# Performance work log

Hardware: AMD Instinct MI355X
Metric: run time of the kernel (lower is better)

The kernel has to match this reference:

```python
import jax, jax.numpy as jnp
import numpy as np
from jax.scipy.special import logsumexp

B, D, H, L, R, K = 4096, 784, 16, 4, 4, 8
D1 = D // 2
NBIS, NNEWT = 50, 3
LOG2PI = float(np.log(2.0 * np.pi))


def square_swish(h):
    # util.square_swish nonlinearity (swish-family; see notes)
    return h * jax.nn.sigmoid(h)


def mixture_terms(xv, logits, mu, log_s):
    # xv: [B, D1]; logits/mu/log_s: [B, D1, K]
    logw = jax.nn.log_softmax(logits, axis=-1)
    t = (xv[..., None] - mu) * jnp.exp(-log_s)
    log_cdf = logsumexp(logw + jax.nn.log_sigmoid(t), axis=-1)          # log F(x)
    log_sf = logsumexp(logw + jax.nn.log_sigmoid(-t), axis=-1)          # log (1-F(x))
    log_pdf = logsumexp(logw + jax.nn.log_sigmoid(t) + jax.nn.log_sigmoid(-t) - log_s, axis=-1)  # log F'(x)
    return log_cdf, log_sf, log_pdf


def invert_mixture_logit(y, logits, mu, log_s):
    # Solve logit(F(x)) = y for x: bisection (stop-grad) + Newton polish (differentiable).
    sl, sm, ss, sy = map(jax.lax.stop_gradient, (logits, mu, log_s, y))

    def body(_, lo_hi):
        lo, hi = lo_hi
        mid = 0.5 * (lo + hi)
        lc, lsf, _ = mixture_terms(mid, sl, sm, ss)
        f = lc - lsf - sy
        return jnp.where(f < 0, mid, lo), jnp.where(f < 0, hi, mid)

    lo = jnp.full_like(y, -100.0)
    hi = jnp.full_like(y, 100.0)
    lo, hi = jax.lax.fori_loop(0, NBIS, body, (lo, hi))
    xv = jax.lax.stop_gradient(0.5 * (lo + hi))
    for _ in range(NNEWT):
        lc, lsf, lp = mixture_terms(xv, logits, mu, log_s)
        logdet = lp - lc - lsf  # d/dx logit(F(x))
        xv = xv - (lc - lsf - y) * jnp.exp(-logdet)
    lc, lsf, lp = mixture_terms(xv, logits, mu, log_s)
    return xv, lp - lc - lsf


def conditioner(h_in, Wi, bi, W1l, b1l, W2l, b2l, Wo, bo):
    h = square_swish(h_in @ Wi + bi)
    for r in range(R):  # 4 resnet blocks, hidden_dim=16
        h = h + square_swish(h @ W1l[r] + b1l[r]) @ W2l[r] + b2l[r]
    return (h @ Wo + bo).reshape(-1, D1, 3 * K)


def flow_inverse(x, eps, W_in, b_in, W1, b1, W2, b2, W_out, b_out):
    # UnitGaussianPrior sample eps -> inverse coupling stack; log q via change of variables
    log_q = -0.5 * jnp.sum(eps * eps + LOG2PI, axis=-1)
    z = eps
    for l in reversed(range(L)):
        za, zb = z[:, :D1], z[:, D1:]
        if l % 2 == 1:
            za, zb = zb, za
        p = conditioner(jnp.concatenate([zb, x], axis=-1),
                        W_in[l], b_in[l], W1[l], b1[l], W2[l], b2[l], W_out[l], b_out[l])
        logits, mu, log_s = p[..., :K], p[..., K:2 * K], p[..., 2 * K:]
        xa, ld = invert_mixture_logit(za, logits, mu, log_s)
        log_q = log_q + jnp.sum(ld, axis=-1)
        if l % 2 == 0:
            z = jnp.concatenate([xa, zb], axis=-1)
        else:
            z = jnp.concatenate([zb, xa], axis=-1)
    return z, log_q


def setup_inputs():
    key = jax.random.key(0)
    ks = jax.random.split(key, 6)
    s_in = 1.0 / np.sqrt(D1 + D)
    s_h = 1.0 / np.sqrt(H)
    return {
        "x": jax.random.normal(ks[0], (B, D), jnp.float32),
        "eps": jax.random.normal(ks[1], (B, D), jnp.float32),
        "W_in": jax.random.normal(ks[2], (L, D1 + D, H), jnp.float32) * s_in,
        "b_in": jnp.zeros((L, H), jnp.float32),
        "W1": jax.random.normal(ks[3], (L, R, H, H), jnp.float32) * s_h,
        "b1": jnp.zeros((L, R, H), jnp.float32),
        "W2": jax.random.normal(ks[4], (L, R, H, H), jnp.float32) * s_h,
        "b2": jnp.zeros((L, R, H), jnp.float32),
        "W_out": jax.random.normal(ks[5], (L, H, D1 * 3 * K), jnp.float32) * 0.05,
        "b_out": jnp.zeros((L, D1 * 3 * K), jnp.float32),
    }


def reference(x, eps, W_in, b_in, W1, b1, W2, b2, W_out, b_out):
    return flow_inverse(x, eps, W_in, b_in, W1, b1, W2, b2, W_out, b_out)
```

## Files before the change

### kernel.cpp

```cpp
#include <hip/hip_runtime.h>
#include <math.h>

constexpr int cB   = 4096;
constexpr int cD   = 784;
constexpr int cD1  = 392;
constexpr int cH   = 16;
constexpr int cL   = 4;
constexpr int cR   = 4;
constexpr int cDIN = 1176;
constexpr int cPDIM = cD1 * 3 * 8;
#define LOG2PI_F 1.8378770664093453f
#define L2E_F    1.4426950408889634f
#define LN2_F    0.6931471805599453f
#define LN_LN2_F (-0.36651292058166432701f)

__device__ __forceinline__ float rcpf(float x)  { return __builtin_amdgcn_rcpf(x); }
__device__ __forceinline__ float exp2f_(float x){ return __builtin_amdgcn_exp2f(x); }
__device__ __forceinline__ float log2f_(float x){ return __builtin_amdgcn_logf(x); }
__device__ __forceinline__ float expn(float x)  { return exp2f_(x * L2E_F); }
__device__ __forceinline__ float logn(float x)  { return log2f_(x) * LN2_F; }

typedef __attribute__((ext_vector_type(2))) float f32x2;

__global__ void __launch_bounds__(256, 4) mlp_kernel(
    const float* __restrict__ zbsrc, const float* __restrict__ x,
    const float* __restrict__ Win, const float* __restrict__ bin,
    const float* __restrict__ W1, const float* __restrict__ b1,
    const float* __restrict__ W2, const float* __restrict__ b2,
    float* __restrict__ hbuf,
    const float* __restrict__ eps, float* __restrict__ logq, int do_init)
{
    __shared__ float part[4][4][16];
    const int wid  = threadIdx.x >> 6;
    const int lane = threadIdx.x & 63;
    const int j = lane & 15;
    const int G = lane >> 4;
    const int bs = blockIdx.x * 4;
    const int r0 = wid * 294;

    if (do_init) {
        const int b = bs + wid;
        const float4* e = (const float4*)(eps + (size_t)b * cD);
        float sum = 0.f;
        for (int i = lane; i < cD / 4; i += 64) {
            float4 v = e[i];
            sum = fmaf(v.x, v.x, sum); sum = fmaf(v.y, v.y, sum);
            sum = fmaf(v.z, v.z, sum); sum = fmaf(v.w, v.w, sum);
        }
        #pragma unroll
        for (int off = 32; off; off >>= 1) sum += __shfl_xor(sum, off, 64);
        if (lane == 0) logq[b] = -0.5f * sum - 0.5f * (float)cD * LOG2PI_F;
    }

    float acc[4][16];
    #pragma unroll
    for (int s = 0; s < 4; ++s)
        #pragma unroll
        for (int c = 0; c < 16; ++c) acc[s][c] = 0.f;

    const float* pz[4]; const float* px[4];
    #pragma unroll
    for (int s = 0; s < 4; ++s) {
        pz[s] = zbsrc + (size_t)(bs + s) * cD;
        px[s] = x + (size_t)(bs + s) * cD - cD1;
    }

    for (int i = r0 + lane; i < r0 + 294; i += 64) {
        const float4* wr = (const float4*)(Win + (size_t)i * cH);
        float4 w0 = wr[0], w1 = wr[1], w2 = wr[2], w3 = wr[3];
        float wv[16] = {w0.x,w0.y,w0.z,w0.w, w1.x,w1.y,w1.z,w1.w,
                        w2.x,w2.y,w2.z,w2.w, w3.x,w3.y,w3.z,w3.w};
        #pragma unroll
        for (int s = 0; s < 4; ++s) {
            const float* src = (i < cD1) ? pz[s] : px[s];
            float v = src[i];
            #pragma unroll
            for (int c = 0; c < 16; ++c) acc[s][c] = fmaf(v, wv[c], acc[s][c]);
        }
    }

    #pragma unroll
    for (int s = 0; s < 4; ++s) {
        #pragma unroll
        for (int c = 0; c < 8; ++c) {
            float sent = (lane & 8) ? acc[s][c] : acc[s][c + 8];
            float mine = (lane & 8) ? acc[s][c + 8] : acc[s][c];
            acc[s][c] = mine + __shfl_xor(sent, 8, 64);
        }
        #pragma unroll
        for (int c = 0; c < 4; ++c) {
            float sent = (lane & 4) ? acc[s][c] : acc[s][c + 4];
            float mine = (lane & 4) ? acc[s][c + 4] : acc[s][c];
            acc[s][c] = mine + __shfl_xor(sent, 4, 64);
        }
        #pragma unroll
        for (int c = 0; c < 2; ++c) {
            float sent = (lane & 2) ? acc[s][c] : acc[s][c + 2];
            float mine = (lane & 2) ? acc[s][c + 2] : acc[s][c];
            acc[s][c] = mine + __shfl_xor(sent, 2, 64);
        }
        {
            float sent = (lane & 1) ? acc[s][0] : acc[s][1];
            float mine = (lane & 1) ? acc[s][1] : acc[s][0];
            acc[s][0] = mine + __shfl_xor(sent, 1, 64);
        }
    }
    const int g4 = (lane >> 4) & 1, g5 = (lane >> 5) & 1;
    float a01, a23, colsum;
    {
        float sent = g4 ? acc[0][0] : acc[1][0];
        float keep = g4 ? acc[1][0] : acc[0][0];
        a01 = keep + __shfl_xor(sent, 16, 64);
    }
    {
        float sent = g4 ? acc[2][0] : acc[3][0];
        float keep = g4 ? acc[3][0] : acc[2][0];
        a23 = keep + __shfl_xor(sent, 16, 64);
    }
    {
        float sent = g5 ? a01 : a23;
        float keep = g5 ? a23 : a01;
        colsum = keep + __shfl_xor(sent, 32, 64);
    }

    part[wid][G][j] = colsum;
    __syncthreads();
    if (wid != 0) return;

    colsum = part[0][G][j] + part[1][G][j] + part[2][G][j] + part[3][G][j];

    float t0 = colsum + bin[j];
    float hj = t0 * rcpf(1.0f + expn(-t0));

    #pragma unroll
    for (int r = 0; r < cR; ++r) {
        const float* w1r = W1 + r * 256;
        const float* w2r = W2 + r * 256;
        float u = b1[r * 16 + j];
        #pragma unroll
        for (int i = 0; i < 16; ++i)
            u = fmaf(__shfl(hj, i, 16), w1r[i * 16 + j], u);
        u = u * rcpf(1.0f + expn(-u));
        float v = b2[r * 16 + j];
        #pragma unroll
        for (int i = 0; i < 16; ++i)
            v = fmaf(__shfl(u, i, 16), w2r[i * 16 + j], v);
        hj += v;
    }
    hbuf[(size_t)j * cB + (bs + G)] = hj;
}

__global__ void __launch_bounds__(256) invert_kernel(
    float* __restrict__ z, const float* __restrict__ ysrc,
    const float* __restrict__ hbuf,
    const float* __restrict__ Wo, const float* __restrict__ bo,
    float* __restrict__ logq, int za_off)
{
    const int wid  = threadIdx.x >> 6;
    const int lane = threadIdx.x & 63;
    const int d = __builtin_amdgcn_readfirstlane(blockIdx.x * 4 + wid);
    const int b = blockIdx.y * 64 + lane;

    float hh[16];
    #pragma unroll
    for (int i = 0; i < 16; ++i) hh[i] = hbuf[(size_t)i * cB + b];

    f32x2 P[12];
    {
        const f32x2* bp = (const f32x2*)(bo + (size_t)d * 24);
        #pragma unroll
        for (int j2 = 0; j2 < 12; ++j2) P[j2] = bp[j2];
        #pragma unroll
        for (int i = 0; i < 16; ++i) {
            float hv = hh[i];
            f32x2 hv2 = {hv, hv};
            const f32x2* wr = (const f32x2*)(Wo + (size_t)i * cPDIM + (size_t)d * 24);
            #pragma unroll
            for (int j2 = 0; j2 < 12; ++j2)
                P[j2] = __builtin_elementwise_fma(hv2, wr[j2], P[j2]);
        }
    }
    float p[24];
    #pragma unroll
    for (int j2 = 0; j2 < 12; ++j2) { p[2*j2] = P[j2].x; p[2*j2+1] = P[j2].y; }

    const float y0  = ysrc[(size_t)b * cD + za_off + d];
    const float sgn = (y0 < 0.f) ? -1.f : 1.f;
    const float yb  = fabsf(y0);

    float wt[8], pm[8], q2[8], is2[8], nm2[8], wis2[8];
    float S, lgSn, SLN2, lo, hi, x0;
    {
        float m = p[0];
        #pragma unroll
        for (int k = 1; k < 8; ++k) m = fmaxf(m, p[k]);
        S = 0.f;
        #pragma unroll
        for (int k = 0; k < 8; ++k) {
            pm[k] = p[k] - m;
            wt[k] = exp2f_(pm[k] * L2E_F);
            S += wt[k];
        }
        lgSn = log2f_(S) * LN2_F;
        SLN2 = S * LN2_F;
        float lo0 = 1e30f, hi0 = -1e30f, xa = 0.f;
        #pragma unroll
        for (int k = 0; k < 8; ++k) {
            q2[k] = p[16 + k] * L2E_F;
            float sk  = exp2f_(q2[k]);
            float ik  = exp2f_(-q2[k]);
            is2[k] = ik * L2E_F;
            float mub = sgn * p[8 + k];
            nm2[k] = -mub * is2[k];
            wis2[k] = wt[k] * is2[k];
            float inv = fmaf(yb, sk, mub);
            lo0 = fminf(lo0, inv); hi0 = fmaxf(hi0, inv);
            xa = fmaf(wt[k], inv, xa);
        }
        float pad = 1e-3f + 1e-5f * (fabsf(lo0) + fabsf(hi0));
        lo = lo0 - pad; hi = hi0 + pad;
        x0 = xa * rcpf(S);
    }

    f32x2 wt2[4], is22[4], nm22[4], wis22[4];
    #pragma unroll
    for (int kk = 0; kk < 4; ++kk) {
        wt2[kk]   = (f32x2){wt[2*kk],   wt[2*kk+1]};
        is22[kk]  = (f32x2){is2[2*kk],  is2[2*kk+1]};
        nm22[kk]  = (f32x2){nm2[2*kk],  nm2[2*kk+1]};
        wis22[kk] = (f32x2){wis2[2*kk], wis2[2*kk+1]};
    }

    float xv, ld;
    if (yb <= 30.0f) {
        xv = x0;
        #pragma unroll 1
        for (int it = 0; it < 3; ++it) {
            f32x2 xv2 = {xv, xv};
            f32x2 sfv2 = {0.f, 0.f}, pdfa2 = {0.f, 0.f};
            #pragma unroll
            for (int kk = 0; kk < 4; ++kk) {
                f32x2 t2 = __builtin_elementwise_fma(xv2, is22[kk], nm22[kk]);
                f32x2 e1;
                e1.x = 1.0f + exp2f_(t2.x);
                e1.y = 1.0f + exp2f_(t2.y);
                f32x2 r = { rcpf(e1.x), rcpf(e1.y) };
                sfv2  = __builtin_elementwise_fma(wt2[kk], r, sfv2);
                f32x2 rr = __builtin_elementwise_fma(-r, r, r);
                pdfa2 = __builtin_elementwise_fma(wis22[kk], rr, pdfa2);
            }
            float sfv = sfv2.x + sfv2.y;
            float pdfa = pdfa2.x + pdfa2.y;
            float cdf = S - sfv;
            float f = (log2f_(cdf) - log2f_(sfv)) * LN2_F;
            if (f < yb) lo = xv; else hi = xv;
            float step = (f - yb) * cdf * sfv * rcpf(pdfa * SLN2);
            float xn = xv - step;
            if (!(xn > lo && xn < hi)) xn = 0.5f * (lo + hi);
            xv = xn;
        }
        {
            f32x2 xv2 = {xv, xv};
            f32x2 sfv2 = {0.f, 0.f}, pdfa2 = {0.f, 0.f};
            #pragma unroll
            for (int kk = 0; kk < 4; ++kk) {
                f32x2 t2 = __builtin_elementwise_fma(xv2, is22[kk], nm22[kk]);
                f32x2 e1;
                e1.x = 1.0f + exp2f_(t2.x);
                e1.y = 1.0f + exp2f_(t2.y);
                f32x2 r = { rcpf(e1.x), rcpf(e1.y) };
                sfv2  = __builtin_elementwise_fma(wt2[kk], r, sfv2);
                f32x2 rr = __builtin_elementwise_fma(-r, r, r);
                pdfa2 = __builtin_elementwise_fma(wis22[kk], rr, pdfa2);
            }
            float sfv = sfv2.x + sfv2.y;
            float pdfa = pdfa2.x + pdfa2.y;
            float cdf = S - sfv;
            float l2c = log2f_(cdf), l2s = log2f_(sfv), l2p = log2f_(pdfa);
            ld = (l2p - l2c - l2s) * LN2_F + LN_LN2_F + lgSn;
            float f = (l2c - l2s) * LN2_F;
            if (f < yb) lo = xv; else hi = xv;
            float step = (f - yb) * cdf * sfv * rcpf(pdfa * SLN2);
            float xn = xv - step;
            if (!(xn > lo && xn < hi)) xn = 0.5f * (lo + hi);
            xv = xn;
        }
    } else {
        float lw[8], lis[8];
        #pragma unroll
        for (int k = 0; k < 8; ++k) {
            lw[k]  = pm[k] - lgSn;
            lis[k] = -q2[k] * LN2_F;
        }
        xv = x0;
        #pragma unroll 1
        for (int it = 0; it < 4; ++it) {
            float u[8];
            float mu_ = -1e30f;
            #pragma unroll
            for (int k = 0; k < 8; ++k) {
                float t  = fmaf(xv, is2[k], nm2[k]) * LN2_F;
                float ec = fminf(expn(-t), 1.0f);
                u[k] = lw[k] - t - ec * fmaf(-0.5f, ec, 1.0f);
                mu_ = fmaxf(mu_, u[k]);
            }
            float Su = 0.f;
            #pragma unroll
            for (int k = 0; k < 8; ++k) Su += expn(u[k] - mu_);
            float lsf = mu_ + logn(Su);
            float m2 = -1e30f;
            #pragma unroll
            for (int k = 0; k < 8; ++k) m2 = fmaxf(m2, u[k] + lis[k]);
            float S2 = 0.f;
            #pragma unroll
            for (int k = 0; k < 8; ++k) S2 += expn(u[k] + lis[k] - m2);
            float lp = m2 + logn(S2);
            if (it == 3) { ld = lp - lsf; break; }
            float f = -lsf;
            if (f < yb) lo = xv; else hi = xv;
            float step = (f - yb) * expn(lsf - lp);
            float xn = xv - step;
            if (!(xn > lo && xn < hi)) xn = 0.5f * (lo + hi);
            xv = xn;
        }
    }

    z[(size_t)b * cD + za_off + d] = sgn * xv;

    __shared__ float red[256];
    red[threadIdx.x] = ld;
    __syncthreads();
    if (wid == 0) {
        float ssum = red[lane] + red[lane + 64] + red[lane + 128] + red[lane + 192];
        atomicAdd(&logq[b], ssum);
    }
}

extern "C" void kernel_launch(void* const* d_in, const int* in_sizes, int n_in,
                              void* d_out, int out_size, void* d_ws, size_t ws_size,
                              hipStream_t stream) {
    const float* x     = (const float*)d_in[0];
    const float* eps   = (const float*)d_in[1];
    const float* W_in  = (const float*)d_in[2];
    const float* b_in  = (const float*)d_in[3];
    const float* W1    = (const float*)d_in[4];
    const float* b1    = (const float*)d_in[5];
    const float* W2    = (const float*)d_in[6];
    const float* b2    = (const float*)d_in[7];
    const float* W_out = (const float*)d_in[8];
    const float* b_out = (const float*)d_in[9];

    float* z    = (float*)d_out;
    float* logq = z + (size_t)cB * cD;
    float* hbuf = (float*)d_ws;

    for (int l = cL - 1; l >= 0; --l) {
        const int zb_off = (l & 1) ? 0 : cD1;
        const int za_off = (l & 1) ? cD1 : 0;
        const float* zbsrc = (l == 3) ? (eps + zb_off) : (z + zb_off);
        const float* ysrc  = (l >= 2) ? eps : z;
        mlp_kernel<<<cB / 4, 256, 0, stream>>>(
            zbsrc, x,
            W_in + (size_t)l * cDIN * cH, b_in + (size_t)l * cH,
            W1 + (size_t)l * cR * cH * cH, b1 + (size_t)l * cR * cH,
            W2 + (size_t)l * cR * cH * cH, b2 + (size_t)l * cR * cH,
            hbuf,
            eps, logq, (l == 3) ? 1 : 0);
        invert_kernel<<<dim3(cD1 / 4, cB / 64), 256, 0, stream>>>(
            z, ysrc, hbuf,
            W_out + (size_t)l * cH * cPDIM, b_out + (size_t)l * cPDIM,
            logq, za_off);
    }
}
```

Measured before the change: 290.7 us.

## Stage Wo tile and hidden activations in shared memory for invert kernel

The invert kernel now loads the block's 16x96 slice of the output weight matrix and the 16x64 hidden-activation tile into LDS cooperatively, then computes the per-lane mixture parameters from LDS using float4 reads. Previously each lane issued redundant global loads for the weights and scattered strided loads for the hidden state. It also recomputes the weight-times-inverse-scale product inside the Newton loop instead of keeping it in registers, which trades a little extra arithmetic for lower register pressure. The added __syncthreads and LDS footprint may reduce occupancy.

```diff
diff --git a/kernel.cpp b/kernel.cpp
--- a/kernel.cpp
+++ b/kernel.cpp
@@ -156,14 +156,35 @@
     const float* __restrict__ Wo, const float* __restrict__ bo,
     float* __restrict__ logq, int za_off)
 {
-    const int wid  = threadIdx.x >> 6;
-    const int lane = threadIdx.x & 63;
+    __shared__ __align__(16) float WoS[16][96];
+    __shared__ float hhS[16][64];
+    __shared__ float red[256];
+
+    const int tid  = threadIdx.x;
+    const int wid  = tid >> 6;
+    const int lane = tid & 63;
+    const int colbase = blockIdx.x * 96;
+    const int b0 = blockIdx.y * 64;
+
+    #pragma unroll
+    for (int t = 0; t < 6; ++t) {
+        int idx = tid + t * 256;
+        int r = idx / 96, c = idx - r * 96;
+        WoS[r][c] = Wo[(size_t)r * cPDIM + colbase + c];
+    }
+    #pragma unroll
+    for (int t = 0; t < 4; ++t) {
+        int idx = tid + t * 256;
+        int i = idx >> 6, bb = idx & 63;
+        hhS[i][bb] = hbuf[(size_t)i * cB + b0 + bb];
+    }
+
     const int d = __builtin_amdgcn_readfirstlane(blockIdx.x * 4 + wid);
-    const int b = blockIdx.y * 64 + lane;
-
-    float hh[16];
-    #pragma unroll
-    for (int i = 0; i < 16; ++i) hh[i] = hbuf[(size_t)i * cB + b];
+    const int b = b0 + lane;
+
+    const float y0  = ysrc[(size_t)b * cD + za_off + d];
+
+    __syncthreads();
 
     f32x2 P[12];
     {
@@ -172,63 +193,59 @@
         for (int j2 = 0; j2 < 12; ++j2) P[j2] = bp[j2];
         #pragma unroll
         for (int i = 0; i < 16; ++i) {
-            float hv = hh[i];
-            f32x2 hv2 = {hv, hv};
-            const f32x2* wr = (const f32x2*)(Wo + (size_t)i * cPDIM + (size_t)d * 24);
-            #pragma unroll
-            for (int j2 = 0; j2 < 12; ++j2)
-                P[j2] = __builtin_elementwise_fma(hv2, wr[j2], P[j2]);
-        }
-    }
-    float p[24];
-    #pragma unroll
-    for (int j2 = 0; j2 < 12; ++j2) { p[2*j2] = P[j2].x; p[2*j2+1] = P[j2].y; }
-
-    const float y0  = ysrc[(size_t)b * cD + za_off + d];
+            const float hv = hhS[i][lane];
+            const f32x2 hv2 = {hv, hv};
+            const float4* wr = (const float4*)&WoS[i][wid * 24];
+            #pragma unroll
+            for (int q = 0; q < 6; ++q) {
+                float4 wv = wr[q];
+                f32x2 wa = {wv.x, wv.y};
+                f32x2 wb = {wv.z, wv.w};
+                P[2*q]   = __builtin_elementwise_fma(hv2, wa, P[2*q]);
+                P[2*q+1] = __builtin_elementwise_fma(hv2, wb, P[2*q+1]);
+            }
+        }
+    }
+
     const float sgn = (y0 < 0.f) ? -1.f : 1.f;
     const float yb  = fabsf(y0);
 
-    float wt[8], pm[8], q2[8], is2[8], nm2[8], wis2[8];
+    f32x2 pm2[4], q22[4], wt2[4], is22[4], nm22[4];
     float S, lgSn, SLN2, lo, hi, x0;
     {
-        float m = p[0];
-        #pragma unroll
-        for (int k = 1; k < 8; ++k) m = fmaxf(m, p[k]);
+        float m = P[0][0];
+        #pragma unroll
+        for (int k = 1; k < 8; ++k) m = fmaxf(m, P[k >> 1][k & 1]);
         S = 0.f;
         #pragma unroll
         for (int k = 0; k < 8; ++k) {
-            pm[k] = p[k] - m;
-            wt[k] = exp2f_(pm[k] * L2E_F);
-            S += wt[k];
+            float pmv = P[k >> 1][k & 1] - m;
+            float wtv = exp2f_(pmv * L2E_F);
+            pm2[k >> 1][k & 1] = pmv;
+            wt2[k >> 1][k & 1] = wtv;
+            S += wtv;
         }
         lgSn = log2f_(S) * LN2_F;
         SLN2 = S * LN2_F;
         float lo0 = 1e30f, hi0 = -1e30f, xa = 0.f;
         #pragma unroll
         for (int k = 0; k < 8; ++k) {
-            q2[k] = p[16 + k] * L2E_F;
-            float sk  = exp2f_(q2[k]);
-            float ik  = exp2f_(-q2[k]);
-            is2[k] = ik * L2E_F;
-            float mub = sgn * p[8 + k];
-            nm2[k] = -mub * is2[k];
-            wis2[k] = wt[k] * is2[k];
+            float q2v = P[8 + (k >> 1)][k & 1] * L2E_F;
+            float sk  = exp2f_(q2v);
+            float ik  = exp2f_(-q2v);
+            float is2v = ik * L2E_F;
+            float mub = sgn * P[4 + (k >> 1)][k & 1];
+            q22[k >> 1][k & 1]  = q2v;
+            is22[k >> 1][k & 1] = is2v;
+            nm22[k >> 1][k & 1] = -mub * is2v;
+            float wtv = wt2[k >> 1][k & 1];
             float inv = fmaf(yb, sk, mub);
             lo0 = fminf(lo0, inv); hi0 = fmaxf(hi0, inv);
-            xa = fmaf(wt[k], inv, xa);
+            xa = fmaf(wtv, inv, xa);
         }
         float pad = 1e-3f + 1e-5f * (fabsf(lo0) + fabsf(hi0));
         lo = lo0 - pad; hi = hi0 + pad;
         x0 = xa * rcpf(S);
-    }
-
-    f32x2 wt2[4], is22[4], nm22[4], wis22[4];
-    #pragma unroll
-    for (int kk = 0; kk < 4; ++kk) {
-        wt2[kk]   = (f32x2){wt[2*kk],   wt[2*kk+1]};
-        is22[kk]  = (f32x2){is2[2*kk],  is2[2*kk+1]};
-        nm22[kk]  = (f32x2){nm2[2*kk],  nm2[2*kk+1]};
-        wis22[kk] = (f32x2){wis2[2*kk], wis2[2*kk+1]};
     }
 
     float xv, ld;
@@ -247,7 +264,8 @@
                 f32x2 r = { rcpf(e1.x), rcpf(e1.y) };
                 sfv2  = __builtin_elementwise_fma(wt2[kk], r, sfv2);
                 f32x2 rr = __builtin_elementwise_fma(-r, r, r);
-                pdfa2 = __builtin_elementwise_fma(wis22[kk], rr, pdfa2);
+                f32x2 wis2v = wt2[kk] * is22[kk];
+                pdfa2 = __builtin_elementwise_fma(wis2v, rr, pdfa2);
             }
             float sfv = sfv2.x + sfv2.y;
             float pdfa = pdfa2.x + pdfa2.y;
@@ -271,7 +289,8 @@
                 f32x2 r = { rcpf(e1.x), rcpf(e1.y) };
                 sfv2  = __builtin_elementwise_fma(wt2[kk], r, sfv2);
                 f32x2 rr = __builtin_elementwise_fma(-r, r, r);
-                pdfa2 = __builtin_elementwise_fma(wis22[kk], rr, pdfa2);
+                f32x2 wis2v = wt2[kk] * is22[kk];
+                pdfa2 = __builtin_elementwise_fma(wis2v, rr, pdfa2);
             }
             float sfv = sfv2.x + sfv2.y;
             float pdfa = pdfa2.x + pdfa2.y;
@@ -286,12 +305,6 @@
             xv = xn;
         }
     } else {
-        float lw[8], lis[8];
-        #pragma unroll
-        for (int k = 0; k < 8; ++k) {
-            lw[k]  = pm[k] - lgSn;
-            lis[k] = -q2[k] * LN2_F;
-        }
         xv = x0;
         #pragma unroll 1
         for (int it = 0; it < 4; ++it) {
@@ -299,9 +312,12 @@
             float mu_ = -1e30f;
             #pragma unroll
             for (int k = 0; k < 8; ++k) {
-                float t  = fmaf(xv, is2[k], nm2[k]) * LN2_F;
+                float is2v = is22[k >> 1][k & 1];
+                float nm2v = nm22[k >> 1][k & 1];
+                float lwv  = pm2[k >> 1][k & 1] - lgSn;
+                float t  = fmaf(xv, is2v, nm2v) * LN2_F;
                 float ec = fminf(expn(-t), 1.0f);
-                u[k] = lw[k] - t - ec * fmaf(-0.5f, ec, 1.0f);
+                u[k] = lwv - t - ec * fmaf(-0.5f, ec, 1.0f);
                 mu_ = fmaxf(mu_, u[k]);
             }
             float Su = 0.f;
@@ -310,10 +326,10 @@
             float lsf = mu_ + logn(Su);
             float m2 = -1e30f;
             #pragma unroll
-            for (int k = 0; k < 8; ++k) m2 = fmaxf(m2, u[k] + lis[k]);
+            for (int k = 0; k < 8; ++k) m2 = fmaxf(m2, u[k] - q22[k >> 1][k & 1] * LN2_F);
             float S2 = 0.f;
             #pragma unroll
-            for (int k = 0; k < 8; ++k) S2 += expn(u[k] + lis[k] - m2);
+            for (int k = 0; k < 8; ++k) S2 += expn(u[k] - q22[k >> 1][k & 1] * LN2_F - m2);
             float lp = m2 + logn(S2);
             if (it == 3) { ld = lp - lsf; break; }
             float f = -lsf;
@@ -327,8 +343,7 @@
 
     z[(size_t)b * cD + za_off + d] = sgn * xv;
 
-    __shared__ float red[256];
-    red[threadIdx.x] = ld;
+    red[tid] = ld;
     __syncthreads();
     if (wid == 0) {
         float ssum = red[lane] + red[lane + 64] + red[lane + 128] + red[lane + 192];
```

After: 297.6 us. 1.02x slower.
